# Performance work log

Measured on AMD Instinct MI355X. Metric: run time of the kernel, lower is better.

Reference implementation:

```python
import jax, jax.numpy as jnp
import numpy as np


def setup_inputs() -> dict:
    key = jax.random.key(0)
    k1, k2, k3 = jax.random.split(key, 3)
    n_nodes, d = 1_000_000, 128
    B, L, w, neg_size = 1024, 80, 5, 4
    A = L - w + 1  # 76 anchors per walk
    walk = jax.random.randint(k1, (B, L), 0, n_nodes)
    # torch.randint(low=1, high=n_nodes-1) -> values in [1, n_nodes-2]
    neg = jax.random.randint(k2, (B, A, neg_size), 1, n_nodes - 1)
    embed = jax.random.normal(k3, (n_nodes, d), dtype=jnp.float32)
    return {"walk": walk, "neg": neg, "embed": embed}


def reference(walk, neg, embed):
    B, L = walk.shape
    A = neg.shape[1]          # L - window_size + 1
    w = L - A + 1             # window_size
    anc = walk[:, :A]                                       # [B, A]
    # pos[b, t, i] = walk[b, t + 1 + i], i in [0, w-2]
    sl = jnp.arange(A)[:, None] + jnp.arange(1, w)[None, :]  # [A, w-1]
    pos = walk[:, sl]                                        # [B, A, w-1]
    e_anc = embed[anc]                                       # [B, A, D]
    # fused gather + per-window dot products
    pos_logit = jnp.einsum('bacd,bad->bac', embed[pos], e_anc)  # [B, A, w-1]
    neg_logit = jnp.einsum('bacd,bad->bac', embed[neg], e_anc)  # [B, A, neg]
    # BCEWithLogitsLoss with labels 1 (pos) and 0 (neg), mean over all elements:
    #   label=1 -> softplus(-x);  label=0 -> softplus(x)
    total = pos_logit.size + neg_logit.size
    loss = (jnp.sum(jax.nn.softplus(-pos_logit)) +
            jnp.sum(jax.nn.softplus(neg_logit))) / total
    return loss
```

## Files before the change

kernel.cpp:

```cpp
#include <hip/hip_runtime.h>
#include <math.h>

#define BD   1024
#define LW   80
#define AA   76
#define NEGS 4
#define D    128
#define PAIRS (BD * AA)
#define WAVES_PER_BLOCK 4
#define NBLOCKS (PAIRS / WAVES_PER_BLOCK)

__device__ __forceinline__ float softplus(float x) {
    return fmaxf(x, 0.0f) + log1pf(__expf(-fabsf(x)));
}

__global__ __launch_bounds__(256, 8) void sg_partial(
    const int* __restrict__ walk, const int* __restrict__ neg,
    const float* __restrict__ embed, float* __restrict__ ws)
{
    __shared__ float s_wsum[WAVES_PER_BLOCK];
    const int tid  = threadIdx.x;
    const int lane = tid & 63;
    const int wave = __builtin_amdgcn_readfirstlane(tid >> 6);
    const int p    = blockIdx.x * WAVES_PER_BLOCK + wave;
    const int b    = p / AA;
    const int a    = p - b * AA;

    const int* wrow = walk + b * LW + a;
    const int anc = wrow[0];
    const int t0  = wrow[1];
    const int t1  = wrow[2];
    const int t2  = wrow[3];
    const int t3  = wrow[4];
    const int4 nv = *(const int4*)(neg + (size_t)p * NEGS);

    const float* erow = embed + (size_t)(lane * 2);
    const float2 ea = *(const float2*)(erow + (size_t)anc  * D);
    const float2 e0 = *(const float2*)(erow + (size_t)t0   * D);
    const float2 e1 = *(const float2*)(erow + (size_t)t1   * D);
    const float2 e2 = *(const float2*)(erow + (size_t)t2   * D);
    const float2 e3 = *(const float2*)(erow + (size_t)t3   * D);
    const float2 e4 = *(const float2*)(erow + (size_t)nv.x * D);
    const float2 e5 = *(const float2*)(erow + (size_t)nv.y * D);
    const float2 e6 = *(const float2*)(erow + (size_t)nv.z * D);
    const float2 e7 = *(const float2*)(erow + (size_t)nv.w * D);

    float a0v = fmaf(ea.x, e0.x, ea.y * e0.y);
    float a1v = fmaf(ea.x, e1.x, ea.y * e1.y);
    float a2v = fmaf(ea.x, e2.x, ea.y * e2.y);
    float a3v = fmaf(ea.x, e3.x, ea.y * e3.y);
    float a4v = fmaf(ea.x, e4.x, ea.y * e4.y);
    float a5v = fmaf(ea.x, e5.x, ea.y * e5.y);
    float a6v = fmaf(ea.x, e6.x, ea.y * e6.y);
    float a7v = fmaf(ea.x, e7.x, ea.y * e7.y);

    const bool hi1 = lane & 1;
    const bool hi2 = lane & 2;
    const bool hi3 = lane & 4;

    float b0 = (hi1 ? a4v : a0v) + __shfl_xor(hi1 ? a0v : a4v, 1);
    float b1 = (hi1 ? a5v : a1v) + __shfl_xor(hi1 ? a1v : a5v, 1);
    float b2 = (hi1 ? a6v : a2v) + __shfl_xor(hi1 ? a2v : a6v, 1);
    float b3 = (hi1 ? a7v : a3v) + __shfl_xor(hi1 ? a3v : a7v, 1);

    float c0 = (hi2 ? b2 : b0) + __shfl_xor(hi2 ? b0 : b2, 2);
    float c1 = (hi2 ? b3 : b1) + __shfl_xor(hi2 ? b1 : b3, 2);

    float dv = (hi3 ? c1 : c0) + __shfl_xor(hi3 ? c0 : c1, 4);
    dv += __shfl_xor(dv, 8);
    dv += __shfl_xor(dv, 16);
    dv += __shfl_xor(dv, 32);

    float v = softplus(hi1 ? dv : -dv);

    #pragma unroll
    for (int m = 1; m < 64; m <<= 1) v += __shfl_xor(v, m);

    if (lane == 0) s_wsum[wave] = v * 0.125f;
    __syncthreads();
    if (tid == 0)
        ws[blockIdx.x] = s_wsum[0] + s_wsum[1] + s_wsum[2] + s_wsum[3];
}

__global__ __launch_bounds__(1024) void sg_reduce(
    const float* __restrict__ ws, float* __restrict__ out)
{
    __shared__ float s[16];
    const int tid = threadIdx.x;
    float sum = 0.0f;
    #pragma unroll
    for (int i = 0; i < NBLOCKS / 1024; ++i)
        sum += ws[tid + i * 1024];
    #pragma unroll
    for (int m = 1; m < 64; m <<= 1) sum += __shfl_xor(sum, m);
    const int wave = tid >> 6;
    const int lane = tid & 63;
    if (lane == 0) s[wave] = sum;
    __syncthreads();
    if (tid == 0) {
        float acc = 0.0f;
        #pragma unroll
        for (int i = 0; i < 16; ++i) acc += s[i];
        const float total = (float)((size_t)PAIRS * 8);
        out[0] = acc * (1.0f / total);
    }
}

extern "C" void kernel_launch(void* const* d_in, const int* in_sizes, int n_in,
                              void* d_out, int out_size, void* d_ws, size_t ws_size,
                              hipStream_t stream) {
    const int*   walk  = (const int*)d_in[0];
    const int*   neg   = (const int*)d_in[1];
    const float* embed = (const float*)d_in[2];
    float* ws  = (float*)d_ws;
    float* out = (float*)d_out;

    sg_partial<<<NBLOCKS, 256, 0, stream>>>(walk, neg, embed, ws);
    sg_reduce<<<1, 1024, 0, stream>>>(ws, out);
}
```

Before: 588.8 us.

## Bucket-sort negative samples by row index and split positive/negative gather kernels

Negative sample indices are counting-sorted into 1024 coarse buckets by row id (histogram, scan, atomic scatter), so the negative-row gathers run in a more address-ordered sequence and can get better DRAM or cache locality. Positive pairs are computed in a separate kernel, and each negative pair now costs one wave that re-gathers its anchor row. The change adds four preprocessing launches and extra workspace traffic, and the scatter's atomic order makes the summation order nondeterministic.

```diff
diff --git a/kernel.cpp b/kernel.cpp
--- a/kernel.cpp
+++ b/kernel.cpp
@@ -7,102 +7,179 @@
 #define NEGS 4
 #define D    128
 #define PAIRS (BD * AA)
-#define WAVES_PER_BLOCK 4
-#define NBLOCKS (PAIRS / WAVES_PER_BLOCK)
+#define NNEG  (PAIRS * NEGS)
+#define NLOGIT ((size_t)PAIRS * 8)
+
+#define NBUCKET 1024
+#define BSHIFT  10
+#define CPAD    16
+
+#define CNT_OFF   0
+#define CUR_OFF   (NBUCKET * CPAD)
+#define REC_OFF_BYTES  (1u << 18)
+#define PART_OFF_BYTES (1u << 22)
+#define POS_BLOCKS 4864
+#define NEG_BLOCKS 19456
+#define NPART (POS_BLOCKS + NEG_BLOCKS)
 
 __device__ __forceinline__ float softplus(float x) {
     return fmaxf(x, 0.0f) + log1pf(__expf(-fabsf(x)));
 }
 
-__global__ __launch_bounds__(256, 8) void sg_partial(
-    const int* __restrict__ walk, const int* __restrict__ neg,
-    const float* __restrict__ embed, float* __restrict__ ws)
-{
-    __shared__ float s_wsum[WAVES_PER_BLOCK];
+
+__global__ __launch_bounds__(1024) void k_zero(int* __restrict__ wsi) {
+    const int i = blockIdx.x * 1024 + threadIdx.x;
+    wsi[i] = 0;
+}
+
+__global__ __launch_bounds__(1024) void k_hist(
+    const int* __restrict__ neg, int* __restrict__ cnt)
+{
+    __shared__ int h[NBUCKET];
+    const int tid = threadIdx.x;
+    h[tid] = 0;
+    __syncthreads();
+    const int beg = blockIdx.x * (NNEG / 64);
+    const int end = beg + (NNEG / 64);
+    for (int i = beg + tid; i < end; i += 1024)
+        atomicAdd(&h[neg[i] >> BSHIFT], 1);
+    __syncthreads();
+    if (h[tid]) atomicAdd(&cnt[tid * CPAD], h[tid]);
+}
+
+__global__ __launch_bounds__(1024) void k_scan(
+    const int* __restrict__ cnt, int* __restrict__ cur)
+{
+    __shared__ int s[NBUCKET];
+    const int tid = threadIdx.x;
+    const int c = cnt[tid * CPAD];
+    s[tid] = c;
+    __syncthreads();
+    for (int off = 1; off < NBUCKET; off <<= 1) {
+        int t = (tid >= off) ? s[tid - off] : 0;
+        __syncthreads();
+        s[tid] += t;
+        __syncthreads();
+    }
+    cur[tid * CPAD] = s[tid] - c;
+}
+
+__global__ __launch_bounds__(1024) void k_scatter(
+    const int* __restrict__ neg, int* __restrict__ cur, int2* __restrict__ rec)
+{
+    const int i = blockIdx.x * 1024 + threadIdx.x;
+    const int idx = neg[i];
+    const int pos = atomicAdd(&cur[(idx >> BSHIFT) * CPAD], 1);
+    rec[pos] = make_int2(idx, i >> 2);
+}
+
+
+__global__ __launch_bounds__(1024) void k_pos(
+    const int* __restrict__ walk, const float* __restrict__ embed,
+    float* __restrict__ part)
+{
+    __shared__ float s[16];
     const int tid  = threadIdx.x;
     const int lane = tid & 63;
     const int wave = __builtin_amdgcn_readfirstlane(tid >> 6);
-    const int p    = blockIdx.x * WAVES_PER_BLOCK + wave;
+    const int p    = blockIdx.x * 16 + wave;
     const int b    = p / AA;
     const int a    = p - b * AA;
 
-    const int* wrow = walk + b * LW + a;
-    const int anc = wrow[0];
-    const int t0  = wrow[1];
-    const int t1  = wrow[2];
-    const int t2  = wrow[3];
-    const int t3  = wrow[4];
-    const int4 nv = *(const int4*)(neg + (size_t)p * NEGS);
+    const int* wr = walk + b * LW + a;
+    const int anc = wr[0], t0 = wr[1], t1 = wr[2], t2 = wr[3], t3 = wr[4];
 
     const float* erow = embed + (size_t)(lane * 2);
-    const float2 ea = *(const float2*)(erow + (size_t)anc  * D);
-    const float2 e0 = *(const float2*)(erow + (size_t)t0   * D);
-    const float2 e1 = *(const float2*)(erow + (size_t)t1   * D);
-    const float2 e2 = *(const float2*)(erow + (size_t)t2   * D);
-    const float2 e3 = *(const float2*)(erow + (size_t)t3   * D);
-    const float2 e4 = *(const float2*)(erow + (size_t)nv.x * D);
-    const float2 e5 = *(const float2*)(erow + (size_t)nv.y * D);
-    const float2 e6 = *(const float2*)(erow + (size_t)nv.z * D);
-    const float2 e7 = *(const float2*)(erow + (size_t)nv.w * D);
-
-    float a0v = fmaf(ea.x, e0.x, ea.y * e0.y);
-    float a1v = fmaf(ea.x, e1.x, ea.y * e1.y);
-    float a2v = fmaf(ea.x, e2.x, ea.y * e2.y);
-    float a3v = fmaf(ea.x, e3.x, ea.y * e3.y);
-    float a4v = fmaf(ea.x, e4.x, ea.y * e4.y);
-    float a5v = fmaf(ea.x, e5.x, ea.y * e5.y);
-    float a6v = fmaf(ea.x, e6.x, ea.y * e6.y);
-    float a7v = fmaf(ea.x, e7.x, ea.y * e7.y);
-
-    const bool hi1 = lane & 1;
-    const bool hi2 = lane & 2;
-    const bool hi3 = lane & 4;
-
-    float b0 = (hi1 ? a4v : a0v) + __shfl_xor(hi1 ? a0v : a4v, 1);
-    float b1 = (hi1 ? a5v : a1v) + __shfl_xor(hi1 ? a1v : a5v, 1);
-    float b2 = (hi1 ? a6v : a2v) + __shfl_xor(hi1 ? a2v : a6v, 1);
-    float b3 = (hi1 ? a7v : a3v) + __shfl_xor(hi1 ? a3v : a7v, 1);
-
-    float c0 = (hi2 ? b2 : b0) + __shfl_xor(hi2 ? b0 : b2, 2);
-    float c1 = (hi2 ? b3 : b1) + __shfl_xor(hi2 ? b1 : b3, 2);
-
-    float dv = (hi3 ? c1 : c0) + __shfl_xor(hi3 ? c0 : c1, 4);
+    const float2 ea = *(const float2*)(erow + (size_t)anc * D);
+    const float2 e0 = *(const float2*)(erow + (size_t)t0  * D);
+    const float2 e1 = *(const float2*)(erow + (size_t)t1  * D);
+    const float2 e2 = *(const float2*)(erow + (size_t)t2  * D);
+    const float2 e3 = *(const float2*)(erow + (size_t)t3  * D);
+
+    float p0 = fmaf(ea.x, e0.x, ea.y * e0.y);
+    float p1 = fmaf(ea.x, e1.x, ea.y * e1.y);
+    float p2 = fmaf(ea.x, e2.x, ea.y * e2.y);
+    float p3 = fmaf(ea.x, e3.x, ea.y * e3.y);
+
+    const bool h1 = lane & 1, h2 = lane & 2;
+    float q0 = (h1 ? p1 : p0) + __shfl_xor(h1 ? p0 : p1, 1);
+    float q1 = (h1 ? p3 : p2) + __shfl_xor(h1 ? p2 : p3, 1);
+    float dv = (h2 ? q1 : q0) + __shfl_xor(h2 ? q0 : q1, 2);
+    dv += __shfl_xor(dv, 4);
     dv += __shfl_xor(dv, 8);
     dv += __shfl_xor(dv, 16);
     dv += __shfl_xor(dv, 32);
 
-    float v = softplus(hi1 ? dv : -dv);
-
-    #pragma unroll
-    for (int m = 1; m < 64; m <<= 1) v += __shfl_xor(v, m);
-
-    if (lane == 0) s_wsum[wave] = v * 0.125f;
-    __syncthreads();
-    if (tid == 0)
-        ws[blockIdx.x] = s_wsum[0] + s_wsum[1] + s_wsum[2] + s_wsum[3];
-}
-
-__global__ __launch_bounds__(1024) void sg_reduce(
-    const float* __restrict__ ws, float* __restrict__ out)
+    float v = softplus(-dv);
+    v += __shfl_xor(v, 1);
+    v += __shfl_xor(v, 2);
+
+    if (lane == 0) s[wave] = v;
+    __syncthreads();
+    if (tid == 0) {
+        float t = 0.f;
+        #pragma unroll
+        for (int i = 0; i < 16; ++i) t += s[i];
+        part[blockIdx.x] = t;
+    }
+}
+
+__global__ __launch_bounds__(1024) void k_neg(
+    const int* __restrict__ walk, const float* __restrict__ embed,
+    const int2* __restrict__ rec, float* __restrict__ part)
+{
+    __shared__ float s[16];
+    const int tid  = threadIdx.x;
+    const int lane = tid & 63;
+    const int wave = __builtin_amdgcn_readfirstlane(tid >> 6);
+    const int rid  = blockIdx.x * 16 + wave;
+
+    const int2 rc = rec[rid];
+    const int idx = __builtin_amdgcn_readfirstlane(rc.x);
+    const int p   = __builtin_amdgcn_readfirstlane(rc.y);
+    const int b   = p / AA;
+    const int a   = p - b * AA;
+    const int anc = walk[b * LW + a];
+
+    const float* erow = embed + (size_t)(lane * 2);
+    const float2 et = *(const float2*)(erow + (size_t)idx * D);
+    const float2 ea = *(const float2*)(erow + (size_t)anc * D);
+
+    float dv = fmaf(et.x, ea.x, et.y * ea.y);
+    dv += __shfl_xor(dv, 1);
+    dv += __shfl_xor(dv, 2);
+    dv += __shfl_xor(dv, 4);
+    dv += __shfl_xor(dv, 8);
+    dv += __shfl_xor(dv, 16);
+    dv += __shfl_xor(dv, 32);
+
+    if (lane == 0) s[wave] = softplus(dv);
+    __syncthreads();
+    if (tid == 0) {
+        float t = 0.f;
+        #pragma unroll
+        for (int i = 0; i < 16; ++i) t += s[i];
+        part[POS_BLOCKS + blockIdx.x] = t;
+    }
+}
+
+__global__ __launch_bounds__(1024) void k_reduce(
+    const float* __restrict__ part, float* __restrict__ out)
 {
     __shared__ float s[16];
     const int tid = threadIdx.x;
-    float sum = 0.0f;
-    #pragma unroll
-    for (int i = 0; i < NBLOCKS / 1024; ++i)
-        sum += ws[tid + i * 1024];
+    float sum = 0.f;
+    for (int i = tid; i < NPART; i += 1024) sum += part[i];
     #pragma unroll
     for (int m = 1; m < 64; m <<= 1) sum += __shfl_xor(sum, m);
-    const int wave = tid >> 6;
-    const int lane = tid & 63;
+    const int wave = tid >> 6, lane = tid & 63;
     if (lane == 0) s[wave] = sum;
     __syncthreads();
     if (tid == 0) {
-        float acc = 0.0f;
+        float acc = 0.f;
         #pragma unroll
         for (int i = 0; i < 16; ++i) acc += s[i];
-        const float total = (float)((size_t)PAIRS * 8);
-        out[0] = acc * (1.0f / total);
+        out[0] = acc * (1.0f / (float)NLOGIT);
     }
 }
 
@@ -112,9 +189,19 @@
     const int*   walk  = (const int*)d_in[0];
     const int*   neg   = (const int*)d_in[1];
     const float* embed = (const float*)d_in[2];
-    float* ws  = (float*)d_ws;
-    float* out = (float*)d_out;
-
-    sg_partial<<<NBLOCKS, 256, 0, stream>>>(walk, neg, embed, ws);
-    sg_reduce<<<1, 1024, 0, stream>>>(ws, out);
-}
+
+    int*   wsi  = (int*)d_ws;
+    int*   cnt  = wsi + CNT_OFF;
+    int*   cur  = wsi + CUR_OFF;
+    int2*  rec  = (int2*)((char*)d_ws + REC_OFF_BYTES);
+    float* part = (float*)((char*)d_ws + PART_OFF_BYTES);
+    float* out  = (float*)d_out;
+
+    k_zero   <<<32,   1024, 0, stream>>>(wsi);
+    k_hist   <<<64,   1024, 0, stream>>>(neg, cnt);
+    k_scan   <<<1,    1024, 0, stream>>>(cnt, cur);
+    k_scatter<<<304,  1024, 0, stream>>>(neg, cur, rec);
+    k_pos    <<<POS_BLOCKS, 1024, 0, stream>>>(walk, embed, part);
+    k_neg    <<<NEG_BLOCKS, 1024, 0, stream>>>(walk, embed, rec, part);
+    k_reduce <<<1,    1024, 0, stream>>>(part, out);
+}
```

After: 701.7 us. 1.19x slower.
